# Optimization experiments

Hardware: AMD Instinct MI355X
Metric: run time of the kernel (lower is better)

## Reference

```python
import jax, jax.numpy as jnp
import numpy as np

B, T, F, C, K = 32, 4096, 128, 256, 128
NEG_HUGE = -1e38


def setup_inputs() -> dict:
    key = jax.random.key(0)
    ks = jax.random.split(key, 9)
    s0 = jax.random.normal(ks[0], (C,), dtype=jnp.float32)
    inp = {
        "x": jax.random.normal(ks[1], (B, T, F), dtype=jnp.float32),
        "n": jnp.zeros((B, C), dtype=jnp.float32),
        "d": jnp.zeros((B, C), dtype=jnp.float32),
        "h": jnp.broadcast_to(jnp.tanh(s0), (B, C)),  # init_internal: h = tanh(s0)
        "a_max": jnp.full((B, C), NEG_HUGE, dtype=jnp.float32),
        # nn.Linear default init scale ~ 1/sqrt(fan_in)
        "g_w": jax.random.normal(ks[2], (C, F + C), dtype=jnp.float32) / np.sqrt(F + C),
        "g_b": jax.random.normal(ks[3], (C,), dtype=jnp.float32) / np.sqrt(F + C),
        "u_w": jax.random.normal(ks[4], (C, F), dtype=jnp.float32) / np.sqrt(F),
        "u_b": jax.random.normal(ks[5], (C,), dtype=jnp.float32) / np.sqrt(F),
        "a_w": jax.random.normal(ks[6], (C, F + C), dtype=jnp.float32) / np.sqrt(F + C),
        "o_w": jax.random.normal(ks[7], (K, C), dtype=jnp.float32) / np.sqrt(C),
        "o_b": jax.random.normal(ks[8], (K,), dtype=jnp.float32) / np.sqrt(C),
    }
    return inp


def reference(x, n, d, h, a_max, g_w, g_b, u_w, u_b, a_w, o_w, o_b):
    def step(carry, x_t):
        n, d, h, a_max = carry  # each [B, C]
        xh = jnp.concatenate([x_t, h], axis=1)          # [B, F+C]
        u_t = x_t @ u_w.T + u_b                          # [B, C]
        g_t = xh @ g_w.T + g_b                           # [B, C]
        a_t = xh @ a_w.T                                 # [B, C] (no bias)
        z_t = u_t * jnp.tanh(g_t)
        a_new = jnp.maximum(a_max, a_t)
        exp_diff = jnp.exp(a_max - a_new)
        exp_scaled = jnp.exp(a_t - a_new)
        n_t = n * exp_diff + z_t * exp_scaled
        d_t = d * exp_diff + exp_scaled
        h_t = jnp.tanh(n_t / d_t)
        out = h_t @ o_w.T + o_b                          # [B, K]
        return (n_t, d_t, h_t, a_new), out

    (n_t, d_t, h_t, a_new), outs = jax.lax.scan(
        step, (n, d, h, a_max), jnp.swapaxes(x, 0, 1))   # scan over time
    outs = jnp.swapaxes(outs, 0, 1)                      # [B, T, K]
    return outs, n_t, d_t, h_t, a_new
```

## Files before the change

### kernel.cpp

```cpp
#include <hip/hip_runtime.h>
#include <hip/hip_fp16.h>

#define B_ 32
#define T_ 4096
#define F_ 128
#define C_ 256
#define K_ 128
#define FC_ 384

typedef __attribute__((ext_vector_type(8))) short s8v;
typedef __attribute__((ext_vector_type(4))) float f4v;
typedef __attribute__((ext_vector_type(4))) int   i4v;

#define MFMA16(a,b,c) __builtin_amdgcn_mfma_f32_16x16x32_bf16((a),(b),(c),0,0,0)
#define MFMAI8(a,b,c) __builtin_amdgcn_mfma_i32_16x16x64_i8((a),(b),(c),0,0,0)

#define LOG2E  1.442695041f
#define LOG2E2 2.885390082f
#define LN2    0.6931471806f

#define WS_WSCAN 0u
#define WS_SMAX  131072u
#define WS_W1F   262144u
#define WS_OWF   458752u
#define WS_BIAS1 524288u
#define WS_CARRY 527360u
#define WS_DYN   658432u

__device__ __forceinline__ unsigned short f2bf(float f){
  unsigned u = __float_as_uint(f);
  u += 0x7fffu + ((u>>16)&1u);
  return (unsigned short)(u>>16);
}
__device__ __forceinline__ float h2f(unsigned short s){
  __half_raw r; r.x = s; return __half2float((__half)r);
}
__device__ __forceinline__ float fexp2(float x){
#if __has_builtin(__builtin_amdgcn_exp2f)
  return __builtin_amdgcn_exp2f(x);
#else
  return __expf(x*0.69314718056f);
#endif
}

__global__ __launch_bounds__(256) void scale_kernel(
    const float* __restrict__ g_w, const float* __restrict__ a_w, char* __restrict__ ws)
{
  int id = blockIdx.x*256 + threadIdx.x;
  if (id >= 512) return;
  const float* src = (id < 256) ? g_w : a_w;
  int c = id & 255;
  float m = 0.0f;
  #pragma unroll 8
  for (int k=0;k<256;++k) m = fmaxf(m, fabsf(src[c*FC_ + F_ + k]));
  ((float*)(ws + WS_SMAX))[id] = fmaxf(m, 1e-30f);
}

__global__ __launch_bounds__(256) void pack_kernel(
    const float* __restrict__ g_w, const float* __restrict__ u_w, const float* __restrict__ a_w,
    const float* __restrict__ g_b, const float* __restrict__ u_b, const float* __restrict__ o_w,
    char* __restrict__ ws)
{
  int id = blockIdx.x*256 + threadIdx.x;
  const float* smax = (const float*)(ws + WS_SMAX);
  unsigned short* w1f   = (unsigned short*)(ws + WS_W1F);
  unsigned short* owf   = (unsigned short*)(ws + WS_OWF);
  float* bias1          = (float*)(ws + WS_BIAS1);
  if (id < 8192){
    int l = id & 63, kc = (id>>6)&3, tp = (id>>8)&3, mat = (id>>10)&1, wv = id>>11;
    int c  = wv*64 + tp*16 + (l&15);
    int kb = kc*64 + (l>>4)*16;
    const float* src = mat ? a_w : g_w;
    float inv = 127.0f / smax[mat*256 + c];
    int w32[4] = {0,0,0,0};
    #pragma unroll
    for (int j=0;j<16;++j){
      int q8 = __float2int_rn(src[c*FC_ + F_ + kb + j] * inv);
      w32[j>>2] |= (q8 & 0xff) << (8*(j&3));
    }
    int* dst = (int*)(ws + WS_WSCAN) + id*4;
    dst[0]=w32[0]; dst[1]=w32[1]; dst[2]=w32[2]; dst[3]=w32[3];
  } else if (id < 8192+12288){
    int id2 = id - 8192;
    int l = id2 & 63, kc = (id2>>6)&3, nt = id2>>8;
    int n = nt*16 + (l&15);
    int kb = kc*32 + (l>>4)*8;
    float sc = (n < 256) ? 1.0f : (n < 512) ? LOG2E2 : LOG2E;
    #pragma unroll
    for (int j=0;j<8;++j){
      int k = kb + j;
      float v = (n < 256) ? u_w[n*F_ + k]
              : (n < 512) ? g_w[(n-256)*FC_ + k]
                          : a_w[(n-512)*FC_ + k];
      w1f[id2*8+j] = f2bf(v*sc);
    }
  } else if (id < 8192+12288+4096){
    int id3 = id - (8192+12288);
    int l = id3 & 63, kc = (id3>>6)&7, nt = id3>>9;
    int n = nt*16 + (l&15);
    int kb = kc*32 + (l>>4)*8;
    #pragma unroll
    for (int j=0;j<8;++j)
      owf[id3*8+j] = f2bf(o_w[n*C_ + kb + j]);
  } else if (id < 8192+12288+4096+768){
    int i = id - (8192+12288+4096);
    bias1[i] = (i<256) ? u_b[i] : (i<512 ? g_b[i-256]*LOG2E2 : 0.0f);
  }
}

__global__ __launch_bounds__(256) void init_kernel(
    const float* __restrict__ n0, const float* __restrict__ d0,
    const float* __restrict__ h0, const float* __restrict__ am0, char* __restrict__ ws)
{
  int id = blockIdx.x*256 + threadIdx.x;
  float* c = (float*)(ws + WS_CARRY);
  c[id]        = n0[id];
  c[8192+id]   = d0[id];
  c[16384+id]  = h0[id];
  c[24576+id]  = am0[id]*LOG2E;
}

__global__ __launch_bounds__(256) void ph1_kernel(const float* __restrict__ x, char* __restrict__ ws,
                                                  int t0, int Tc, int lgT16)
{
  const s8v* w1f = (const s8v*)(ws + WS_W1F);
  const float* bias1 = (const float*)(ws + WS_BIAS1);
  __half* pre = (__half*)(ws + WS_DYN);
  int tid = threadIdx.x;
  int wv = tid>>6, l = tid&63, q = l>>4, col = l&15;
  int wid = blockIdx.x*4 + wv;
  int b  = wid >> lgT16;
  int tb = (wid & ((1<<lgT16)-1))*16;
  s8v af[4];
  const float* xr = x + ((size_t)b*T_ + t0 + tb + col)*F_ + q*8;
  #pragma unroll
  for (int kc=0;kc<4;++kc){
    const float* p = xr + kc*32;
    float4 p0 = *(const float4*)(p);
    float4 p1 = *(const float4*)(p+4);
    s8v a;
    a[0]=(short)f2bf(p0.x); a[1]=(short)f2bf(p0.y); a[2]=(short)f2bf(p0.z); a[3]=(short)f2bf(p0.w);
    a[4]=(short)f2bf(p1.x); a[5]=(short)f2bf(p1.y); a[6]=(short)f2bf(p1.z); a[7]=(short)f2bf(p1.w);
    af[kc]=a;
  }
  for (int nt=0;nt<48;++nt){
    f4v acc = {0.f,0.f,0.f,0.f};
    #pragma unroll
    for (int kc=0;kc<4;++kc)
      acc = MFMA16(af[kc], w1f[(nt*4+kc)*64 + l], acc);
    int cg = nt*16 + col;
    float bs = bias1[cg];
    #pragma unroll
    for (int i=0;i<4;++i){
      int rl = tb + q*4 + i;
      pre[(size_t)(b*Tc + rl)*768 + cg] = __float2half(acc[i] + bs);
    }
  }
}

__global__ __launch_bounds__(256,1) void scan_kernel(char* __restrict__ ws, int Tc)
{
  __shared__ __align__(16) char h8buf[2][256];
  const i4v* wp = (const i4v*)(ws + WS_WSCAN);
  const float* smax = (const float*)(ws + WS_SMAX);
  const unsigned short* prbu = (const unsigned short*)(ws + WS_DYN);
  unsigned short* hall = (unsigned short*)(ws + WS_DYN + 49152u*(unsigned)Tc);
  float* carry = (float*)(ws + WS_CARRY);
  int tid = threadIdx.x;
  int wv = tid>>6, l = tid&63, q = l>>4, col = l&15;
  int b = blockIdx.x;
  int c = wv*64 + q*16 + col;

  i4v wg[4][4], wa[4][4];
  #pragma unroll
  for (int tp=0;tp<4;++tp)
    #pragma unroll
    for (int kc=0;kc<4;++kc){
      wg[tp][kc] = wp[(((wv*2+0)*4+tp)*4+kc)*64 + l];
      wa[tp][kc] = wp[(((wv*2+1)*4+tp)*4+kc)*64 + l];
    }
  float gsc = smax[c]     * (LOG2E2/16129.0f);
  float asc = smax[256+c] * (LOG2E /16129.0f);

  int gi = b*C_ + c;
  float cn = carry[gi], cd = carry[8192+gi], cm = carry[24576+gi];
  h8buf[0][c] = (char)__float2int_rn(carry[16384+gi]*127.0f);
  __syncthreads();

  const size_t prb = (size_t)b*Tc*768;
  unsigned short* hrow = hall + (size_t)b*Tc*C_ + c;

  unsigned short su[4], sg[4], sa[4];
  #pragma unroll
  for (int i=0;i<4;++i){
    size_t o = prb + (size_t)i*768;
    su[i]=prbu[o + c]; sg[i]=prbu[o + 256+c]; sa[i]=prbu[o + 512+c];
  }

  #pragma unroll 1
  for (int t=0;t<Tc;t+=4){
    #pragma unroll
    for (int ph=0; ph<4; ++ph){
      int s = t + ph;
      const char* hc = h8buf[ph&1];
      char* hn = h8buf[(ph&1)^1];
      i4v aG[4], aA[4];
      #pragma unroll
      for (int tp=0;tp<4;++tp){ aG[tp]=(i4v){0,0,0,0}; aA[tp]=(i4v){0,0,0,0}; }
      #pragma unroll
      for (int kc=0;kc<4;++kc){
        i4v af = *(const i4v*)(hc + kc*64 + q*16);
        #pragma unroll
        for (int tp=0;tp<4;++tp){
          aG[tp]=MFMAI8(af,wg[tp][kc],aG[tp]);
          aA[tp]=MFMAI8(af,wa[tp][kc],aA[tp]);
        }
      }
      float fu = h2f(su[ph]), fg = h2f(sg[ph]), fa = h2f(sa[ph]);
      {
        int nxt = (s+4 < Tc) ? s+4 : s;
        size_t o = prb + (size_t)nxt*768;
        su[ph]=prbu[o + c]; sg[ph]=prbu[o + 256+c]; sa[ph]=prbu[o + 512+c];
      }
      int g01 = (q&1)? aG[1][0] : aG[0][0];
      int g23 = (q&1)? aG[3][0] : aG[2][0];
      float g = (float)((q&2)? g23 : g01) * gsc + fg;
      int a01 = (q&1)? aA[1][0] : aA[0][0];
      int a23 = (q&1)? aA[3][0] : aA[2][0];
      float a = (float)((q&2)? a23 : a01) * asc + fa;

      float z = fu * (1.0f - 2.0f*__builtin_amdgcn_rcpf(fexp2(g) + 1.0f));
      float anew = fmaxf(cm,a);
      float dmin = fminf(cm,a);
      float e = fexp2(dmin-anew);
      bool ge = (a>=cm);
      float ed = ge? e : 1.0f;
      float es = ge? 1.0f : e;
      cn = cn*ed + z*es;
      cd = fmaf(cd,ed,es);
      float hv = 1.0f - 2.0f*__builtin_amdgcn_rcpf(fexp2(LOG2E2*(cn*__builtin_amdgcn_rcpf(cd))) + 1.0f);
      cm = anew;
      hn[c] = (char)__float2int_rn(hv*127.0f);
      hrow[(size_t)s*C_] = f2bf(hv);
      asm volatile("s_waitcnt lgkmcnt(0)" ::: "memory");
      __builtin_amdgcn_s_barrier();
      asm volatile("" ::: "memory");
    }
  }
  carry[gi] = cn; carry[8192+gi] = cd; carry[24576+gi] = cm;
  carry[16384+gi] = 1.0f - 2.0f*__builtin_amdgcn_rcpf(fexp2(LOG2E2*(cn*__builtin_amdgcn_rcpf(cd))) + 1.0f);
}

__global__ __launch_bounds__(256) void ph3_kernel(const float* __restrict__ o_b,
                                                  char* __restrict__ ws, float* __restrict__ out,
                                                  int t0, int Tc, int lgT16)
{
  const s8v* owf = (const s8v*)(ws + WS_OWF);
  const unsigned short* hall = (const unsigned short*)(ws + WS_DYN + 49152u*(unsigned)Tc);
  int tid = threadIdx.x;
  int wv = tid>>6, l = tid&63, q=l>>4, col=l&15;
  int wid = blockIdx.x*4 + wv;
  int bb = wid >> lgT16;
  int tt = (wid & ((1<<lgT16)-1))*16;
  const unsigned short* src = hall + ((size_t)bb*Tc + tt)*C_;
  s8v af[8];
  #pragma unroll
  for (int kc=0;kc<8;++kc)
    af[kc] = *(const s8v*)(src + (size_t)col*C_ + kc*32 + q*8);
  #pragma unroll
  for (int nt=0;nt<8;++nt){
    f4v acc={0.f,0.f,0.f,0.f};
    #pragma unroll
    for (int kc=0;kc<8;++kc)
      acc = MFMA16(af[kc], owf[(nt*8+kc)*64 + l], acc);
    int k = nt*16+col;
    float bs = o_b[k];
    #pragma unroll
    for (int i=0;i<4;++i)
      out[((size_t)bb*T_ + t0 + tt + q*4 + i)*K_ + k] = acc[i] + bs;
  }
}

__global__ __launch_bounds__(256) void fin_kernel(char* __restrict__ ws, float* __restrict__ out)
{
  int id = blockIdx.x*256 + threadIdx.x;
  const float* c = (const float*)(ws + WS_CARRY);
  size_t ob = (size_t)B_*T_*K_;
  out[ob + id]         = c[id];
  out[ob + 8192 + id]  = c[8192+id];
  out[ob + 16384 + id] = c[16384+id];
  out[ob + 24576 + id] = c[24576+id]*LN2;
}

extern "C" void kernel_launch(void* const* d_in, const int* in_sizes, int n_in,
                              void* d_out, int out_size, void* d_ws, size_t ws_size,
                              hipStream_t stream)
{
  const float* x   = (const float*)d_in[0];
  const float* n0  = (const float*)d_in[1];
  const float* d0  = (const float*)d_in[2];
  const float* h0  = (const float*)d_in[3];
  const float* am0 = (const float*)d_in[4];
  const float* g_w = (const float*)d_in[5];
  const float* g_b = (const float*)d_in[6];
  const float* u_w = (const float*)d_in[7];
  const float* u_b = (const float*)d_in[8];
  const float* a_w = (const float*)d_in[9];
  const float* o_w = (const float*)d_in[10];
  const float* o_b = (const float*)d_in[11];
  float* out = (float*)d_out;
  char* ws = (char*)d_ws;

  unsigned Tc = 4096;
  while (Tc > 64 && (size_t)WS_DYN + 65536ull*Tc > ws_size) Tc >>= 1;
  if ((size_t)WS_DYN + 65536ull*Tc > ws_size) return;
  int lgTc  = __builtin_ctz(Tc);
  int lgT16 = lgTc - 4;
  int nch   = T_ / (int)Tc;

  hipLaunchKernelGGL(scale_kernel, dim3(2), dim3(256), 0, stream, g_w, a_w, ws);
  hipLaunchKernelGGL(pack_kernel, dim3(99), dim3(256), 0, stream,
                     g_w, u_w, a_w, g_b, u_b, o_w, ws);
  hipLaunchKernelGGL(init_kernel, dim3(32), dim3(256), 0, stream,
                     n0, d0, h0, am0, ws);
  for (int c0=0; c0<nch; ++c0){
    int t0 = c0*(int)Tc;
    hipLaunchKernelGGL(ph1_kernel, dim3(B_*(int)Tc/64), dim3(256), 0, stream,
                       x, ws, t0, (int)Tc, lgT16);
    hipLaunchKernelGGL(scan_kernel, dim3(B_), dim3(256), 0, stream,
                       ws, (int)Tc);
    hipLaunchKernelGGL(ph3_kernel, dim3(B_*(int)Tc/64), dim3(256), 0, stream,
                       o_b, ws, out, t0, (int)Tc, lgT16);
  }
  hipLaunchKernelGGL(fin_kernel, dim3(32), dim3(256), 0, stream, ws, out);
}
```

Measured before the change: 2.131 ms.

## Replace per-step int8 MFMA recurrence matvec with per-thread sdot4 dot products

The recurrent h·W matvec in the scan loop switches from int8 MFMA tiles, where only diagonal entries were used, to each thread computing its own column with packed 4-way int8 dot instructions. Weights are repacked so each thread holds its column's 256 int8 weights for both the g and a matrices in registers, and h is read from LDS as broadcast vectors. This removes the wasted MFMA work and the MFMA dependency latency on the serial critical path. In exchange it issues many VALU dot instructions and LDS broadcast reads per step.

```diff
diff --git a/kernel.cpp b/kernel.cpp
--- a/kernel.cpp
+++ b/kernel.cpp
@@ -13,7 +13,6 @@
 typedef __attribute__((ext_vector_type(4))) int   i4v;
 
 #define MFMA16(a,b,c) __builtin_amdgcn_mfma_f32_16x16x32_bf16((a),(b),(c),0,0,0)
-#define MFMAI8(a,b,c) __builtin_amdgcn_mfma_i32_16x16x64_i8((a),(b),(c),0,0,0)
 
 #define LOG2E  1.442695041f
 #define LOG2E2 2.885390082f
@@ -40,6 +39,18 @@
   return __builtin_amdgcn_exp2f(x);
 #else
   return __expf(x*0.69314718056f);
+#endif
+}
+__device__ __forceinline__ int dot4(int a, int b, int c){
+#if __has_builtin(__builtin_amdgcn_sdot4)
+  return __builtin_amdgcn_sdot4(a, b, c, false);
+#else
+  int r = c;
+  r += (int)(char)(a      ) * (int)(char)(b      );
+  r += (int)(char)(a >> 8 ) * (int)(char)(b >> 8 );
+  r += (int)(char)(a >> 16) * (int)(char)(b >> 16);
+  r += (int)(char)(a >> 24) * (int)(char)(b >> 24);
+  return r;
 #endif
 }
 
@@ -67,18 +78,18 @@
   unsigned short* owf   = (unsigned short*)(ws + WS_OWF);
   float* bias1          = (float*)(ws + WS_BIAS1);
   if (id < 8192){
-    int l = id & 63, kc = (id>>6)&3, tp = (id>>8)&3, mat = (id>>10)&1, wv = id>>11;
-    int c  = wv*64 + tp*16 + (l&15);
-    int kb = kc*64 + (l>>4)*16;
+    int i4 = id & 15, mc = id >> 4;
+    int c = mc & 255, mat = mc >> 8;
     const float* src = mat ? a_w : g_w;
     float inv = 127.0f / smax[mat*256 + c];
     int w32[4] = {0,0,0,0};
     #pragma unroll
     for (int j=0;j<16;++j){
-      int q8 = __float2int_rn(src[c*FC_ + F_ + kb + j] * inv);
+      int k = i4*16 + j;
+      int q8 = __float2int_rn(src[c*FC_ + F_ + k] * inv);
       w32[j>>2] |= (q8 & 0xff) << (8*(j&3));
     }
-    int* dst = (int*)(ws + WS_WSCAN) + id*4;
+    int* dst = (int*)(ws + WS_WSCAN) + mc*64 + i4*4;
     dst[0]=w32[0]; dst[1]=w32[1]; dst[2]=w32[2]; dst[3]=w32[3];
   } else if (id < 8192+12288){
     int id2 = id - 8192;
@@ -171,14 +182,12 @@
   int b = blockIdx.x;
   int c = wv*64 + q*16 + col;
 
-  i4v wg[4][4], wa[4][4];
-  #pragma unroll
-  for (int tp=0;tp<4;++tp)
-    #pragma unroll
-    for (int kc=0;kc<4;++kc){
-      wg[tp][kc] = wp[(((wv*2+0)*4+tp)*4+kc)*64 + l];
-      wa[tp][kc] = wp[(((wv*2+1)*4+tp)*4+kc)*64 + l];
-    }
+  i4v wgr[16], war[16];
+  #pragma unroll
+  for (int i=0;i<16;++i){
+    wgr[i] = wp[(size_t)c*16 + i];
+    war[i] = wp[(size_t)(256 + c)*16 + i];
+  }
   float gsc = smax[c]     * (LOG2E2/16129.0f);
   float asc = smax[256+c] * (LOG2E /16129.0f);
 
@@ -204,17 +213,20 @@
       int s = t + ph;
       const char* hc = h8buf[ph&1];
       char* hn = h8buf[(ph&1)^1];
-      i4v aG[4], aA[4];
+      const i4v* hv4 = (const i4v*)hc;
+      int ag0=0, ag1=0, ag2=0, ag3=0;
+      int aa0=0, aa1=0, aa2=0, aa3=0;
       #pragma unroll
-      for (int tp=0;tp<4;++tp){ aG[tp]=(i4v){0,0,0,0}; aA[tp]=(i4v){0,0,0,0}; }
-      #pragma unroll
-      for (int kc=0;kc<4;++kc){
-        i4v af = *(const i4v*)(hc + kc*64 + q*16);
-        #pragma unroll
-        for (int tp=0;tp<4;++tp){
-          aG[tp]=MFMAI8(af,wg[tp][kc],aG[tp]);
-          aA[tp]=MFMAI8(af,wa[tp][kc],aA[tp]);
-        }
+      for (int i=0;i<16;++i){
+        i4v h4 = hv4[i];
+        ag0 = dot4(h4[0], wgr[i][0], ag0);
+        ag1 = dot4(h4[1], wgr[i][1], ag1);
+        ag2 = dot4(h4[2], wgr[i][2], ag2);
+        ag3 = dot4(h4[3], wgr[i][3], ag3);
+        aa0 = dot4(h4[0], war[i][0], aa0);
+        aa1 = dot4(h4[1], war[i][1], aa1);
+        aa2 = dot4(h4[2], war[i][2], aa2);
+        aa3 = dot4(h4[3], war[i][3], aa3);
       }
       float fu = h2f(su[ph]), fg = h2f(sg[ph]), fa = h2f(sa[ph]);
       {
@@ -222,12 +234,8 @@
         size_t o = prb + (size_t)nxt*768;
         su[ph]=prbu[o + c]; sg[ph]=prbu[o + 256+c]; sa[ph]=prbu[o + 512+c];
       }
-      int g01 = (q&1)? aG[1][0] : aG[0][0];
-      int g23 = (q&1)? aG[3][0] : aG[2][0];
-      float g = (float)((q&2)? g23 : g01) * gsc + fg;
-      int a01 = (q&1)? aA[1][0] : aA[0][0];
-      int a23 = (q&1)? aA[3][0] : aA[2][0];
-      float a = (float)((q&2)? a23 : a01) * asc + fa;
+      float g = (float)((ag0+ag1)+(ag2+ag3)) * gsc + fg;
+      float a = (float)((aa0+aa1)+(aa2+aa3)) * asc + fa;
 
       float z = fu * (1.0f - 2.0f*__builtin_amdgcn_rcpf(fexp2(g) + 1.0f));
       float anew = fmaxf(cm,a);
```

After: 3.881 ms. +82.1%, slower.
